# Optimization experiments

Measured on AMD Instinct MI355X. Metric: run time of the kernel, lower is better.

The kernel has to match this reference:

```python
import jax, jax.numpy as jnp
import numpy as np

B, N, H = 8, 256, 256


def setup_inputs() -> dict:
    key = jax.random.key(0)
    ks = jax.random.split(key, 6)
    s = 1.0 / np.sqrt(H)
    return {
        "x": jax.random.normal(ks[0], (B, N, H), dtype=jnp.float32),
        "edge_gate": jax.random.uniform(ks[1], (B, N, N, H), dtype=jnp.float32),
        "U_w": jax.random.uniform(ks[2], (H, H), jnp.float32, -s, s),
        "U_b": jax.random.uniform(ks[3], (H,), jnp.float32, -s, s),
        "V_w": jax.random.uniform(ks[4], (H, H), jnp.float32, -s, s),
        "V_b": jax.random.uniform(ks[5], (H,), jnp.float32, -s, s),
    }


def reference(x, edge_gate, U_w, U_b, V_w, V_b):
    # Ux, Vx: (B, N, H); torch Linear computes x @ W.T + b
    Ux = jnp.einsum("bnh,kh->bnk", x, U_w) + U_b
    Vx = jnp.einsum("bnh,kh->bnk", x, V_w) + V_b
    # sum_j edge_gate[b,i,j,h] * Vx[b,j,h]  -> (B, N, H), fused (no gateVx materialized)
    num = jnp.einsum("bijh,bjh->bih", edge_gate, Vx)
    denom = 1e-20 + jnp.sum(edge_gate, axis=2)  # (B, N, H)
    return Ux + num / denom
```

## Files before the change

kernel.cpp:

```cpp
#include <hip/hip_runtime.h>


typedef float f4 __attribute__((ext_vector_type(4)));
typedef float f2 __attribute__((ext_vector_type(2)));

#define S36 36

__global__ __launch_bounds__(256) void gemm_uv(
    const float* __restrict__ x, const float* __restrict__ U_w,
    const float* __restrict__ U_b, const float* __restrict__ V_w,
    const float* __restrict__ V_b, float* __restrict__ Ux,
    float* __restrict__ Vx) {
  __shared__ float Xs[64 * S36];
  __shared__ float Ws[32 * S36];
  const int t  = threadIdx.x;
  const int gx = blockIdx.x;
  const int gy = blockIdx.y;
  const int m0 = gy * 64;
  const bool isU = (gx < 8);
  const float* Wsrc = isU ? U_w : V_w;
  const float* bsrc = isU ? U_b : V_b;
  const int n0 = (gx & 7) * 32;
  float* dst = isU ? Ux : Vx;

  const int tn = t & 15;
  const int tm = t >> 4;
  float acc[4][2] = {};

  const int lm = t >> 3;
  const int lc = t & 7;

  for (int k0 = 0; k0 < 256; k0 += 32) {
    #pragma unroll
    for (int r = 0; r < 2; ++r) {
      const int m = r * 32 + lm;
      f4 v = *(const f4*)(x + (m0 + m) * 256 + k0 + lc * 4);
      *(f4*)(&Xs[m * S36 + lc * 4]) = v;
    }
    {
      f4 v = *(const f4*)(Wsrc + (n0 + lm) * 256 + k0 + lc * 4);
      *(f4*)(&Ws[lm * S36 + lc * 4]) = v;
    }
    __syncthreads();
    #pragma unroll
    for (int kq = 0; kq < 8; ++kq) {
      f4 a0 = *(const f4*)(&Xs[(tm * 4 + 0) * S36 + kq * 4]);
      f4 a1 = *(const f4*)(&Xs[(tm * 4 + 1) * S36 + kq * 4]);
      f4 a2 = *(const f4*)(&Xs[(tm * 4 + 2) * S36 + kq * 4]);
      f4 a3 = *(const f4*)(&Xs[(tm * 4 + 3) * S36 + kq * 4]);
      f4 b0 = *(const f4*)(&Ws[(tn * 2 + 0) * S36 + kq * 4]);
      f4 b1 = *(const f4*)(&Ws[(tn * 2 + 1) * S36 + kq * 4]);
      acc[0][0] += a0.x*b0.x + a0.y*b0.y + a0.z*b0.z + a0.w*b0.w;
      acc[0][1] += a0.x*b1.x + a0.y*b1.y + a0.z*b1.z + a0.w*b1.w;
      acc[1][0] += a1.x*b0.x + a1.y*b0.y + a1.z*b0.z + a1.w*b0.w;
      acc[1][1] += a1.x*b1.x + a1.y*b1.y + a1.z*b1.z + a1.w*b1.w;
      acc[2][0] += a2.x*b0.x + a2.y*b0.y + a2.z*b0.z + a2.w*b0.w;
      acc[2][1] += a2.x*b1.x + a2.y*b1.y + a2.z*b1.z + a2.w*b1.w;
      acc[3][0] += a3.x*b0.x + a3.y*b0.y + a3.z*b0.z + a3.w*b0.w;
      acc[3][1] += a3.x*b1.x + a3.y*b1.y + a3.z*b1.z + a3.w*b1.w;
    }
    __syncthreads();
  }

  const float bb0 = bsrc[n0 + 2 * tn + 0];
  const float bb1 = bsrc[n0 + 2 * tn + 1];
  #pragma unroll
  for (int i = 0; i < 4; ++i) {
    f2 o;
    o.x = acc[i][0] + bb0;
    o.y = acc[i][1] + bb1;
    *(f2*)(dst + (m0 + 4 * tm + i) * 256 + n0 + 2 * tn) = o;
  }
}

__global__ __launch_bounds__(256) void fuse_gate(
    const float* __restrict__ eg, const float* __restrict__ Vx,
    float* __restrict__ out) {
  const int t    = threadIdx.x;
  const int lane = t & 63;
  const int w    = t >> 6;
  const int row  = blockIdx.x * 4 + w;
  const int b    = row >> 8;

  const f4* eg4 = (const f4*)eg + (size_t)row * (256 * 64) + lane;
  const f4* vx4 = (const f4*)Vx + (size_t)b   * (256 * 64) + lane;

  f4 n0 = {0.f, 0.f, 0.f, 0.f}, n1 = {0.f, 0.f, 0.f, 0.f};
  f4 d0 = {0.f, 0.f, 0.f, 0.f}, d1 = {0.f, 0.f, 0.f, 0.f};

  #pragma unroll 1
  for (int j = 0; j < 256; j += 8) {
    const f4* ep = eg4 + j * 64;
    const f4* vp = vx4 + j * 64;
    f4 e0 = __builtin_nontemporal_load(ep + 0 * 64);
    f4 e1 = __builtin_nontemporal_load(ep + 1 * 64);
    f4 e2 = __builtin_nontemporal_load(ep + 2 * 64);
    f4 e3 = __builtin_nontemporal_load(ep + 3 * 64);
    f4 e4 = __builtin_nontemporal_load(ep + 4 * 64);
    f4 e5 = __builtin_nontemporal_load(ep + 5 * 64);
    f4 e6 = __builtin_nontemporal_load(ep + 6 * 64);
    f4 e7 = __builtin_nontemporal_load(ep + 7 * 64);
    f4 v0 = vp[0 * 64];
    f4 v1 = vp[1 * 64];
    f4 v2 = vp[2 * 64];
    f4 v3 = vp[3 * 64];
    f4 v4 = vp[4 * 64];
    f4 v5 = vp[5 * 64];
    f4 v6 = vp[6 * 64];
    f4 v7 = vp[7 * 64];
    n0 += e0 * v0;  d0 += e0;
    n1 += e1 * v1;  d1 += e1;
    n0 += e2 * v2;  d0 += e2;
    n1 += e3 * v3;  d1 += e3;
    n0 += e4 * v4;  d0 += e4;
    n1 += e5 * v5;  d1 += e5;
    n0 += e6 * v6;  d0 += e6;
    n1 += e7 * v7;  d1 += e7;
  }

  const f4 num = n0 + n1;
  const f4 den = d0 + d1;
  const size_t o = (size_t)row * 64 + lane;
  f4 u = ((const f4*)out)[o];
  f4 eps = {1e-20f, 1e-20f, 1e-20f, 1e-20f};
  ((f4*)out)[o] = u + num / (eps + den);
}

extern "C" void kernel_launch(void* const* d_in, const int* in_sizes, int n_in,
                              void* d_out, int out_size, void* d_ws, size_t ws_size,
                              hipStream_t stream) {
  const float* x   = (const float*)d_in[0];
  const float* eg  = (const float*)d_in[1];
  const float* U_w = (const float*)d_in[2];
  const float* U_b = (const float*)d_in[3];
  const float* V_w = (const float*)d_in[4];
  const float* V_b = (const float*)d_in[5];
  float* out = (float*)d_out;
  float* Vx  = (float*)d_ws;

  gemm_uv<<<dim3(16, 32), 256, 0, stream>>>(x, U_w, U_b, V_w, V_b, out, Vx);
  fuse_gate<<<dim3(512), 256, 0, stream>>>(eg, Vx, out);
}
```

Before: 668.1 us.

## Fuse U/V projections into gated aggregation kernel with per-block Vx recompute

```diff
diff --git a/kernel.cpp b/kernel.cpp
--- a/kernel.cpp
+++ b/kernel.cpp
@@ -2,128 +2,154 @@
 
 
 typedef float f4 __attribute__((ext_vector_type(4)));
-typedef float f2 __attribute__((ext_vector_type(2)));
 
-#define S36 36
+#define NF4 64
 
-__global__ __launch_bounds__(256) void gemm_uv(
-    const float* __restrict__ x, const float* __restrict__ U_w,
-    const float* __restrict__ U_b, const float* __restrict__ V_w,
-    const float* __restrict__ V_b, float* __restrict__ Ux,
-    float* __restrict__ Vx) {
-  __shared__ float Xs[64 * S36];
-  __shared__ float Ws[32 * S36];
-  const int t  = threadIdx.x;
-  const int gx = blockIdx.x;
-  const int gy = blockIdx.y;
-  const int m0 = gy * 64;
-  const bool isU = (gx < 8);
-  const float* Wsrc = isU ? U_w : V_w;
-  const float* bsrc = isU ? U_b : V_b;
-  const int n0 = (gx & 7) * 32;
-  float* dst = isU ? Ux : Vx;
-
-  const int tn = t & 15;
-  const int tm = t >> 4;
-  float acc[4][2] = {};
-
-  const int lm = t >> 3;
-  const int lc = t & 7;
-
-  for (int k0 = 0; k0 < 256; k0 += 32) {
-    #pragma unroll
-    for (int r = 0; r < 2; ++r) {
-      const int m = r * 32 + lm;
-      f4 v = *(const f4*)(x + (m0 + m) * 256 + k0 + lc * 4);
-      *(f4*)(&Xs[m * S36 + lc * 4]) = v;
-    }
-    {
-      f4 v = *(const f4*)(Wsrc + (n0 + lm) * 256 + k0 + lc * 4);
-      *(f4*)(&Ws[lm * S36 + lc * 4]) = v;
-    }
-    __syncthreads();
-    #pragma unroll
-    for (int kq = 0; kq < 8; ++kq) {
-      f4 a0 = *(const f4*)(&Xs[(tm * 4 + 0) * S36 + kq * 4]);
-      f4 a1 = *(const f4*)(&Xs[(tm * 4 + 1) * S36 + kq * 4]);
-      f4 a2 = *(const f4*)(&Xs[(tm * 4 + 2) * S36 + kq * 4]);
-      f4 a3 = *(const f4*)(&Xs[(tm * 4 + 3) * S36 + kq * 4]);
-      f4 b0 = *(const f4*)(&Ws[(tn * 2 + 0) * S36 + kq * 4]);
-      f4 b1 = *(const f4*)(&Ws[(tn * 2 + 1) * S36 + kq * 4]);
-      acc[0][0] += a0.x*b0.x + a0.y*b0.y + a0.z*b0.z + a0.w*b0.w;
-      acc[0][1] += a0.x*b1.x + a0.y*b1.y + a0.z*b1.z + a0.w*b1.w;
-      acc[1][0] += a1.x*b0.x + a1.y*b0.y + a1.z*b0.z + a1.w*b0.w;
-      acc[1][1] += a1.x*b1.x + a1.y*b1.y + a1.z*b1.z + a1.w*b1.w;
-      acc[2][0] += a2.x*b0.x + a2.y*b0.y + a2.z*b0.z + a2.w*b0.w;
-      acc[2][1] += a2.x*b1.x + a2.y*b1.y + a2.z*b1.z + a2.w*b1.w;
-      acc[3][0] += a3.x*b0.x + a3.y*b0.y + a3.z*b0.z + a3.w*b0.w;
-      acc[3][1] += a3.x*b1.x + a3.y*b1.y + a3.z*b1.z + a3.w*b1.w;
-    }
-    __syncthreads();
-  }
-
-  const float bb0 = bsrc[n0 + 2 * tn + 0];
-  const float bb1 = bsrc[n0 + 2 * tn + 1];
-  #pragma unroll
-  for (int i = 0; i < 4; ++i) {
-    f2 o;
-    o.x = acc[i][0] + bb0;
-    o.y = acc[i][1] + bb1;
-    *(f2*)(dst + (m0 + 4 * tm + i) * 256 + n0 + 2 * tn) = o;
-  }
+__device__ __forceinline__ f4 shfl_xor_f4(f4 v, int m) {
+  f4 r;
+  r.x = __shfl_xor(v.x, m, 64);
+  r.y = __shfl_xor(v.y, m, 64);
+  r.z = __shfl_xor(v.z, m, 64);
+  r.w = __shfl_xor(v.w, m, 64);
+  return r;
 }
 
-__global__ __launch_bounds__(256) void fuse_gate(
-    const float* __restrict__ eg, const float* __restrict__ Vx,
+__global__ __launch_bounds__(512, 4) void node_fused(
+    const float* __restrict__ x, const float* __restrict__ eg,
+    const float* __restrict__ U_w, const float* __restrict__ U_b,
+    const float* __restrict__ V_w, const float* __restrict__ V_b,
     float* __restrict__ out) {
-  const int t    = threadIdx.x;
+  __shared__ float Vxs[256][64];
+
+  const int t  = threadIdx.x;
+  const int hq = blockIdx.x;
+  const int it = blockIdx.y;
+  const int b  = blockIdx.z;
+
+  const f4* x4  = (const f4*)x;
+  const f4* Vw4 = (const f4*)V_w;
+  const f4* Uw4 = (const f4*)U_w;
+
+  {
+    const int jq = t >> 3;
+    const int hg = t & 7;
+    const int j0 = jq * 4;
+    const int hrow = hq * 64 + hg * 8;
+
+    float acc[4][8] = {};
+    const f4* xb = x4 + (size_t)(b * 256 + j0) * NF4;
+    const f4* vb = Vw4 + (size_t)hrow * NF4;
+    for (int k4 = 0; k4 < 64; ++k4) {
+      f4 xa0 = xb[0 * NF4 + k4];
+      f4 xa1 = xb[1 * NF4 + k4];
+      f4 xa2 = xb[2 * NF4 + k4];
+      f4 xa3 = xb[3 * NF4 + k4];
+      #pragma unroll
+      for (int c = 0; c < 8; ++c) {
+        f4 w = vb[c * NF4 + k4];
+        acc[0][c] += xa0.x * w.x + xa0.y * w.y + xa0.z * w.z + xa0.w * w.w;
+        acc[1][c] += xa1.x * w.x + xa1.y * w.y + xa1.z * w.z + xa1.w * w.w;
+        acc[2][c] += xa2.x * w.x + xa2.y * w.y + xa2.z * w.z + xa2.w * w.w;
+        acc[3][c] += xa3.x * w.x + xa3.y * w.y + xa3.z * w.z + xa3.w * w.w;
+      }
+    }
+    const f4* Vb4 = (const f4*)V_b;
+    const f4 bia = Vb4[(hrow >> 2) + 0];
+    const f4 bib = Vb4[(hrow >> 2) + 1];
+    #pragma unroll
+    for (int r = 0; r < 4; ++r) {
+      f4 lo = {acc[r][0] + bia.x, acc[r][1] + bia.y,
+               acc[r][2] + bia.z, acc[r][3] + bia.w};
+      f4 hi = {acc[r][4] + bib.x, acc[r][5] + bib.y,
+               acc[r][6] + bib.z, acc[r][7] + bib.w};
+      *(f4*)&Vxs[j0 + r][hg * 8 + 0] = lo;
+      *(f4*)&Vxs[j0 + r][hg * 8 + 4] = hi;
+    }
+  }
+  __syncthreads();
+
   const int lane = t & 63;
   const int w    = t >> 6;
-  const int row  = blockIdx.x * 4 + w;
-  const int b    = row >> 8;
+  const int jsub = lane >> 4;
+  const int h4   = lane & 15;
 
-  const f4* eg4 = (const f4*)eg + (size_t)row * (256 * 64) + lane;
-  const f4* vx4 = (const f4*)Vx + (size_t)b   * (256 * 64) + lane;
+  const f4* Ub4 = (const f4*)U_b;
+  const f4 ubias = Ub4[hq * 16 + h4];
 
-  f4 n0 = {0.f, 0.f, 0.f, 0.f}, n1 = {0.f, 0.f, 0.f, 0.f};
-  f4 d0 = {0.f, 0.f, 0.f, 0.f}, d1 = {0.f, 0.f, 0.f, 0.f};
+  #pragma unroll
+  for (int ii = 0; ii < 2; ++ii) {
+    const int i = it * 16 + w * 2 + ii;
+    const f4* egp = (const f4*)eg +
+        (size_t)(b * 256 + i) * 256 * NF4 + (size_t)(hq * 16 + h4);
+    const int jb = jsub * 64;
 
-  #pragma unroll 1
-  for (int j = 0; j < 256; j += 8) {
-    const f4* ep = eg4 + j * 64;
-    const f4* vp = vx4 + j * 64;
-    f4 e0 = __builtin_nontemporal_load(ep + 0 * 64);
-    f4 e1 = __builtin_nontemporal_load(ep + 1 * 64);
-    f4 e2 = __builtin_nontemporal_load(ep + 2 * 64);
-    f4 e3 = __builtin_nontemporal_load(ep + 3 * 64);
-    f4 e4 = __builtin_nontemporal_load(ep + 4 * 64);
-    f4 e5 = __builtin_nontemporal_load(ep + 5 * 64);
-    f4 e6 = __builtin_nontemporal_load(ep + 6 * 64);
-    f4 e7 = __builtin_nontemporal_load(ep + 7 * 64);
-    f4 v0 = vp[0 * 64];
-    f4 v1 = vp[1 * 64];
-    f4 v2 = vp[2 * 64];
-    f4 v3 = vp[3 * 64];
-    f4 v4 = vp[4 * 64];
-    f4 v5 = vp[5 * 64];
-    f4 v6 = vp[6 * 64];
-    f4 v7 = vp[7 * 64];
-    n0 += e0 * v0;  d0 += e0;
-    n1 += e1 * v1;  d1 += e1;
-    n0 += e2 * v2;  d0 += e2;
-    n1 += e3 * v3;  d1 += e3;
-    n0 += e4 * v4;  d0 += e4;
-    n1 += e5 * v5;  d1 += e5;
-    n0 += e6 * v6;  d0 += e6;
-    n1 += e7 * v7;  d1 += e7;
+    f4 n0 = {0.f, 0.f, 0.f, 0.f}, n1 = {0.f, 0.f, 0.f, 0.f};
+    f4 d0 = {0.f, 0.f, 0.f, 0.f}, d1 = {0.f, 0.f, 0.f, 0.f};
+
+    #pragma unroll 1
+    for (int jj = 0; jj < 64; jj += 8) {
+      const f4* ep = egp + (size_t)(jb + jj) * NF4;
+      f4 e0 = ep[0 * NF4];
+      f4 e1 = ep[1 * NF4];
+      f4 e2 = ep[2 * NF4];
+      f4 e3 = ep[3 * NF4];
+      f4 e4 = ep[4 * NF4];
+      f4 e5 = ep[5 * NF4];
+      f4 e6 = ep[6 * NF4];
+      f4 e7 = ep[7 * NF4];
+      f4 v0 = *(const f4*)&Vxs[jb + jj + 0][h4 * 4];
+      f4 v1 = *(const f4*)&Vxs[jb + jj + 1][h4 * 4];
+      f4 v2 = *(const f4*)&Vxs[jb + jj + 2][h4 * 4];
+      f4 v3 = *(const f4*)&Vxs[jb + jj + 3][h4 * 4];
+      f4 v4 = *(const f4*)&Vxs[jb + jj + 4][h4 * 4];
+      f4 v5 = *(const f4*)&Vxs[jb + jj + 5][h4 * 4];
+      f4 v6 = *(const f4*)&Vxs[jb + jj + 6][h4 * 4];
+      f4 v7 = *(const f4*)&Vxs[jb + jj + 7][h4 * 4];
+      n0 += e0 * v0;  d0 += e0;
+      n1 += e1 * v1;  d1 += e1;
+      n0 += e2 * v2;  d0 += e2;
+      n1 += e3 * v3;  d1 += e3;
+      n0 += e4 * v4;  d0 += e4;
+      n1 += e5 * v5;  d1 += e5;
+      n0 += e6 * v6;  d0 += e6;
+      n1 += e7 * v7;  d1 += e7;
+    }
+    f4 num = n0 + n1;
+    f4 den = d0 + d1;
+    num += shfl_xor_f4(num, 16);
+    den += shfl_xor_f4(den, 16);
+    num += shfl_xor_f4(num, 32);
+    den += shfl_xor_f4(den, 32);
+
+    f4 ux = {0.f, 0.f, 0.f, 0.f};
+    {
+      const f4* xi = x4 + (size_t)(b * 256 + i) * NF4 + jsub * 16;
+      const f4* u0 = Uw4 + (size_t)(hq * 64 + h4 * 4 + 0) * NF4 + jsub * 16;
+      const f4* u1 = Uw4 + (size_t)(hq * 64 + h4 * 4 + 1) * NF4 + jsub * 16;
+      const f4* u2 = Uw4 + (size_t)(hq * 64 + h4 * 4 + 2) * NF4 + jsub * 16;
+      const f4* u3 = Uw4 + (size_t)(hq * 64 + h4 * 4 + 3) * NF4 + jsub * 16;
+      #pragma unroll 4
+      for (int k4 = 0; k4 < 16; ++k4) {
+        f4 xv = xi[k4];
+        f4 w0 = u0[k4];
+        f4 w1 = u1[k4];
+        f4 w2 = u2[k4];
+        f4 w3 = u3[k4];
+        ux.x += xv.x * w0.x + xv.y * w0.y + xv.z * w0.z + xv.w * w0.w;
+        ux.y += xv.x * w1.x + xv.y * w1.y + xv.z * w1.z + xv.w * w1.w;
+        ux.z += xv.x * w2.x + xv.y * w2.y + xv.z * w2.z + xv.w * w2.w;
+        ux.w += xv.x * w3.x + xv.y * w3.y + xv.z * w3.z + xv.w * w3.w;
+      }
+    }
+    ux += shfl_xor_f4(ux, 16);
+    ux += shfl_xor_f4(ux, 32);
+
+    if (jsub == 0) {
+      f4 eps = {1e-20f, 1e-20f, 1e-20f, 1e-20f};
+      f4 o = ux + ubias + num / (eps + den);
+      ((f4*)out)[(size_t)(b * 256 + i) * NF4 + hq * 16 + h4] = o;
+    }
   }
-
-  const f4 num = n0 + n1;
-  const f4 den = d0 + d1;
-  const size_t o = (size_t)row * 64 + lane;
-  f4 u = ((const f4*)out)[o];
-  f4 eps = {1e-20f, 1e-20f, 1e-20f, 1e-20f};
-  ((f4*)out)[o] = u + num / (eps + den);
 }
 
 extern "C" void kernel_launch(void* const* d_in, const int* in_sizes, int n_in,
@@ -136,8 +162,7 @@
   const float* V_w = (const float*)d_in[4];
   const float* V_b = (const float*)d_in[5];
   float* out = (float*)d_out;
-  float* Vx  = (float*)d_ws;
+  (void)d_ws; (void)ws_size;
 
-  gemm_uv<<<dim3(16, 32), 256, 0, stream>>>(x, U_w, U_b, V_w, V_b, out, Vx);
-  fuse_gate<<<dim3(512), 256, 0, stream>>>(eg, Vx, out);
+  node_fused<<<dim3(4, 16, 8), 512, 0, stream>>>(x, eg, U_w, U_b, V_w, V_b, out);
 }
```

Measured after the change: 980.6 us. 46.8% more time.

## Split gate reduction over j into partial blocks with separate combine kernel

Applied to the files above, without the earlier changes.

```diff
diff --git a/kernel.cpp b/kernel.cpp
--- a/kernel.cpp
+++ b/kernel.cpp
@@ -73,41 +73,43 @@
   }
 }
 
-__global__ __launch_bounds__(256) void fuse_gate(
+__global__ __launch_bounds__(256) void fuse_partial(
     const float* __restrict__ eg, const float* __restrict__ Vx,
-    float* __restrict__ out) {
+    float* __restrict__ part) {
   const int t    = threadIdx.x;
   const int lane = t & 63;
   const int w    = t >> 6;
-  const int row  = blockIdx.x * 4 + w;
+  const int jc   = blockIdx.x;
+  const int row  = blockIdx.y;
   const int b    = row >> 8;
+  const int jb   = jc * 64 + w * 16;
 
-  const f4* eg4 = (const f4*)eg + (size_t)row * (256 * 64) + lane;
-  const f4* vx4 = (const f4*)Vx + (size_t)b   * (256 * 64) + lane;
+  const f4* ep = (const f4*)eg + ((size_t)row * 256 + jb) * 64 + lane;
+  const f4* vp = (const f4*)Vx + ((size_t)b   * 256 + jb) * 64 + lane;
 
-  f4 n0 = {0.f, 0.f, 0.f, 0.f}, n1 = {0.f, 0.f, 0.f, 0.f};
-  f4 d0 = {0.f, 0.f, 0.f, 0.f}, d1 = {0.f, 0.f, 0.f, 0.f};
+  f4 n0 = {0.f,0.f,0.f,0.f}, n1 = {0.f,0.f,0.f,0.f};
+  f4 d0 = {0.f,0.f,0.f,0.f}, d1 = {0.f,0.f,0.f,0.f};
 
-  #pragma unroll 1
-  for (int j = 0; j < 256; j += 8) {
-    const f4* ep = eg4 + j * 64;
-    const f4* vp = vx4 + j * 64;
-    f4 e0 = __builtin_nontemporal_load(ep + 0 * 64);
-    f4 e1 = __builtin_nontemporal_load(ep + 1 * 64);
-    f4 e2 = __builtin_nontemporal_load(ep + 2 * 64);
-    f4 e3 = __builtin_nontemporal_load(ep + 3 * 64);
-    f4 e4 = __builtin_nontemporal_load(ep + 4 * 64);
-    f4 e5 = __builtin_nontemporal_load(ep + 5 * 64);
-    f4 e6 = __builtin_nontemporal_load(ep + 6 * 64);
-    f4 e7 = __builtin_nontemporal_load(ep + 7 * 64);
-    f4 v0 = vp[0 * 64];
-    f4 v1 = vp[1 * 64];
-    f4 v2 = vp[2 * 64];
-    f4 v3 = vp[3 * 64];
-    f4 v4 = vp[4 * 64];
-    f4 v5 = vp[5 * 64];
-    f4 v6 = vp[6 * 64];
-    f4 v7 = vp[7 * 64];
+  #pragma unroll
+  for (int h = 0; h < 2; ++h) {
+    const f4* e8 = ep + h * 8 * 64;
+    const f4* v8 = vp + h * 8 * 64;
+    f4 e0 = __builtin_nontemporal_load(&e8[0 * 64]);
+    f4 e1 = __builtin_nontemporal_load(&e8[1 * 64]);
+    f4 e2 = __builtin_nontemporal_load(&e8[2 * 64]);
+    f4 e3 = __builtin_nontemporal_load(&e8[3 * 64]);
+    f4 e4 = __builtin_nontemporal_load(&e8[4 * 64]);
+    f4 e5 = __builtin_nontemporal_load(&e8[5 * 64]);
+    f4 e6 = __builtin_nontemporal_load(&e8[6 * 64]);
+    f4 e7 = __builtin_nontemporal_load(&e8[7 * 64]);
+    f4 v0 = v8[0 * 64];
+    f4 v1 = v8[1 * 64];
+    f4 v2 = v8[2 * 64];
+    f4 v3 = v8[3 * 64];
+    f4 v4 = v8[4 * 64];
+    f4 v5 = v8[5 * 64];
+    f4 v6 = v8[6 * 64];
+    f4 v7 = v8[7 * 64];
     n0 += e0 * v0;  d0 += e0;
     n1 += e1 * v1;  d1 += e1;
     n0 += e2 * v2;  d0 += e2;
@@ -117,13 +119,39 @@
     n0 += e6 * v6;  d0 += e6;
     n1 += e7 * v7;  d1 += e7;
   }
+  const f4 ns = n0 + n1;
+  const f4 ds = d0 + d1;
 
-  const f4 num = n0 + n1;
-  const f4 den = d0 + d1;
-  const size_t o = (size_t)row * 64 + lane;
-  f4 u = ((const f4*)out)[o];
+  __shared__ f4 sh[8][64];
+  sh[w][lane]     = ns;
+  sh[4 + w][lane] = ds;
+  __syncthreads();
+
+  if (t < 64) {
+    f4 n = sh[0][t] + sh[1][t] + sh[2][t] + sh[3][t];
+    f4 d = sh[4][t] + sh[5][t] + sh[6][t] + sh[7][t];
+    f4* p = (f4*)part + (size_t)(row * 4 + jc) * 128;
+    p[t]      = n;
+    p[64 + t] = d;
+  }
+}
+
+__global__ __launch_bounds__(256) void combine(
+    const float* __restrict__ part, float* __restrict__ out) {
+  const int idx  = blockIdx.x * 256 + threadIdx.x;
+  const int row  = idx >> 6;
+  const int lane = idx & 63;
+  const f4* p = (const f4*)part + (size_t)row * 4 * 128;
+  f4 n = {0.f,0.f,0.f,0.f};
+  f4 d = {0.f,0.f,0.f,0.f};
+  #pragma unroll
+  for (int jc = 0; jc < 4; ++jc) {
+    n += p[jc * 128 + lane];
+    d += p[jc * 128 + 64 + lane];
+  }
+  f4 u = ((const f4*)out)[idx];
   f4 eps = {1e-20f, 1e-20f, 1e-20f, 1e-20f};
-  ((f4*)out)[o] = u + num / (eps + den);
+  ((f4*)out)[idx] = u + n / (eps + d);
 }
 
 extern "C" void kernel_launch(void* const* d_in, const int* in_sizes, int n_in,
@@ -135,9 +163,11 @@
   const float* U_b = (const float*)d_in[3];
   const float* V_w = (const float*)d_in[4];
   const float* V_b = (const float*)d_in[5];
-  float* out = (float*)d_out;
-  float* Vx  = (float*)d_ws;
+  float* out  = (float*)d_out;
+  float* Vx   = (float*)d_ws;
+  float* part = (float*)d_ws + 2048 * 256;
 
   gemm_uv<<<dim3(16, 32), 256, 0, stream>>>(x, U_w, U_b, V_w, V_b, out, Vx);
-  fuse_gate<<<dim3(512), 256, 0, stream>>>(eg, Vx, out);
+  fuse_partial<<<dim3(4, 2048), 256, 0, stream>>>(eg, Vx, part);
+  combine<<<dim3(512), 256, 0, stream>>>(part, out);
 }
```

New measurement: 688.8 us. 1.03x slower.
